# Optimization experiments

Measured on AMD Instinct MI355X. Metric: run time of the kernel, lower is better.

Reference implementation:

```python
import jax, jax.numpy as jnp
import numpy as np
from jax import lax

S = 20      # max_segments
D = 1000    # traj_dict entries
L = 200     # dmp_traj_length
CONV_OUT = 512 * 4 * 4  # 8192 for 100x100 input


def _conv(x, w, b):
    # NCHW valid conv, kernel 3x3, stride 1 (matches nn.Conv2d defaults)
    y = lax.conv_general_dilated(x, w, (1, 1), 'VALID',
                                 dimension_numbers=('NCHW', 'OIHW', 'NCHW'))
    return y + b[None, :, None, None]


def _pool2(x):
    # max_pool2d(kernel=2, stride=2), floor mode == VALID reduce_window
    return lax.reduce_window(x, -jnp.inf, lax.max, (1, 1, 2, 2), (1, 1, 2, 2), 'VALID')


def setup_inputs() -> dict:
    key = jax.random.key(0)
    ks = jax.random.split(key, 20)
    f32 = jnp.float32

    def rn(k, shape, s):
        return jax.random.normal(k, shape, dtype=f32) * s

    x = jax.random.normal(ks[0], (128, 3, 100, 100), dtype=f32)
    w1 = rn(ks[1], (64, 3, 3, 3), 0.1);    b1 = jnp.zeros((64,), f32)
    w2 = rn(ks[2], (128, 64, 3, 3), 0.04); b2 = jnp.zeros((128,), f32)
    w3 = rn(ks[3], (256, 128, 3, 3), 0.03); b3 = jnp.zeros((256,), f32)
    w4 = rn(ks[4], (512, 256, 3, 3), 0.02); b4 = jnp.zeros((512,), f32)
    out_size = 2 + 3 * S
    fw1 = rn(ks[5], (CONV_OUT, 2048), 0.01); fb1 = jnp.zeros((2048,), f32)
    fw2 = rn(ks[6], (2048, 2048), 0.02);     fb2 = jnp.zeros((2048,), f32)
    fw3 = rn(ks[7], (2048, out_size), 0.02); fb3 = jnp.zeros((out_size,), f32)
    traj_dict = jax.random.normal(ks[8], (D, L, 2), dtype=f32)
    return {
        'x': x,
        'w1': w1, 'b1': b1, 'w2': w2, 'b2': b2,
        'w3': w3, 'b3': b3, 'w4': w4, 'b4': b4,
        'fw1': fw1, 'fb1': fb1, 'fw2': fw2, 'fb2': fb2,
        'fw3': fw3, 'fb3': fb3,
        'traj_dict': traj_dict,
    }


def _forward(x, w1, b1, w2, b2, w3, b3, w4, b4,
             fw1, fb1, fw2, fb2, fw3, fb3, traj_dict):
    # conv encoder (relu(maxpool(conv)) x4, matching the torch order)
    h = jax.nn.relu(_pool2(_conv(x, w1, b1)))
    h = jax.nn.relu(_pool2(_conv(h, w2, b2)))
    h = jax.nn.relu(_pool2(_conv(h, w3, b3)))
    h = jax.nn.relu(_pool2(_conv(h, w4, b4)))
    h = h.reshape(h.shape[0], -1)                      # [B, 8192]
    # FC stack: tanh on hidden layers, linear head (dropout p=0 / eval)
    h = jnp.tanh(h @ fw1 + fb1)
    h = jnp.tanh(h @ fw2 + fb2)
    p = h @ fw3 + fb3                                  # [B, 2 + 3S]

    B = p.shape[0]
    init_pos = p[:, :2]                                # [B, 2]
    seg = p[:, 2:].reshape(B, S, 3)                    # (dict_idx, x_scale, y_scale)

    # getTrajFromDict: the loop of round/clamp/sign/abs one-hot masks is exactly
    # a gather at the clamped rounded index (round is half-to-even in both torch and jax)
    idx = jnp.clip(jnp.round(seg[..., 0]), 0, D - 1).astype(jnp.int32)  # [B, S]
    base = traj_dict[idx]                              # [B, S, L, 2]

    scaled = base * seg[:, :, None, 1:3]               # [B, S, L, 2]
    # chain segments: each segment starts at previous segment's endpoint
    offsets = scaled[:, :, -1, :]                      # [B, S, 2]
    starts = init_pos[:, None, :] + jnp.cumsum(offsets, axis=1) - offsets  # exclusive cumsum
    traj = (scaled + starts[:, :, None, :]).reshape(B, S * L, 2)
    return traj


def reference(x, w1, b1, w2, b2, w3, b3, w4, b4,
              fw1, fb1, fw2, fb2, fw3, fb3, traj_dict):
    return _forward(x, w1, b1, w2, b2, w3, b3, w4, b4,
                    fw1, fb1, fw2, fb2, fw3, fb3, traj_dict)
```

## Files before the change

### kernel.cpp

```cpp
#include <hip/hip_runtime.h>
#include <hip/hip_bf16.h>

typedef __attribute__((ext_vector_type(8))) short s8v;
typedef __attribute__((ext_vector_type(4))) float f4v;
typedef unsigned short ushort;
typedef unsigned int uint;

union V8 { s8v v; short s[8]; };

__device__ __forceinline__ short f2bf(float v){
    union { __hip_bfloat16 b; short u; } x;
    x.b = __float2bfloat16(v);
    return x.u;
}
__device__ __forceinline__ float bf2f(short u){
    union { short u; __hip_bfloat16 b; } x;
    x.u = u;
    return __bfloat162float(x.b);
}
__device__ __forceinline__ void splitf(float v, short& h, short& l){
    h = f2bf(v);
    l = f2bf(v - bf2f(h));
}
__device__ __forceinline__ uint packsplit(float v){
    short h, l; splitf(v, h, l);
    return (uint)(ushort)h | ((uint)(ushort)l << 16);
}

template<int CIN, int HIN, int PH, int OCB, int SPT, int OCS, int CICH, int COUT>
__global__ __launch_bounds__(SPT*OCS) void k_conv_pool_relu(
    const float* __restrict__ in, const float* __restrict__ w,
    const float* __restrict__ bias, uint* __restrict__ out)
{
    constexpr int BT    = SPT * OCS;
    constexpr int WIN   = HIN;
    constexpr int PW    = PH;
    constexpr int OCBLK = OCB * OCS;
    constexpr int WSTR  = CICH * 9 + 1;

    __shared__ float wsh[OCBLK * WSTR];

    const int b   = blockIdx.z;
    const int oc0 = blockIdx.y * OCBLK;
    const int t   = threadIdx.x;
    const int spl = (OCS == 1) ? t : (t % SPT);
    const int ocq = (OCS == 1) ? 0 : (t / SPT);
    const int sp  = blockIdx.x * SPT + spl;
    const bool active = sp < PH * PW;
    const int py = active ? (sp / PW) : 0;
    const int px = active ? (sp % PW) : 0;

    float acc[OCB][4];
#pragma unroll
    for (int j = 0; j < OCB; ++j)
        acc[j][0] = acc[j][1] = acc[j][2] = acc[j][3] = 0.f;

    const float* inb = in + (size_t)b * CIN * HIN * WIN;

    for (int c0 = 0; c0 < CIN; c0 += CICH) {
        __syncthreads();
        for (int i = t; i < OCBLK * CICH * 9; i += BT) {
            int j = i / (CICH * 9);
            int r = i - j * (CICH * 9);
            wsh[j * WSTR + r] = w[((size_t)(oc0 + j) * CIN + c0) * 9 + r];
        }
        __syncthreads();

        for (int ci = 0; ci < CICH; ++ci) {
            const float* inc = inb + (size_t)(c0 + ci) * HIN * WIN
                             + (2 * py) * WIN + 2 * px;
            float patch[4][4];
#pragma unroll
            for (int r = 0; r < 4; ++r)
#pragma unroll
                for (int c = 0; c < 4; ++c)
                    patch[r][c] = inc[r * WIN + c];

#pragma unroll
            for (int j = 0; j < OCB; ++j) {
                const float* wp = &wsh[(ocq * OCB + j) * WSTR + ci * 9];
#pragma unroll
                for (int kh = 0; kh < 3; ++kh)
#pragma unroll
                    for (int kw = 0; kw < 3; ++kw) {
                        float wv = wp[kh * 3 + kw];
                        acc[j][0] = fmaf(patch[kh][kw],         wv, acc[j][0]);
                        acc[j][1] = fmaf(patch[kh][kw + 1],     wv, acc[j][1]);
                        acc[j][2] = fmaf(patch[kh + 1][kw],     wv, acc[j][2]);
                        acc[j][3] = fmaf(patch[kh + 1][kw + 1], wv, acc[j][3]);
                    }
            }
        }
    }

    if (active) {
#pragma unroll
        for (int j = 0; j < OCB; ++j) {
            int oc = oc0 + ocq * OCB + j;
            float m = fmaxf(fmaxf(acc[j][0], acc[j][1]),
                            fmaxf(acc[j][2], acc[j][3]));
            m = fmaxf(m + bias[oc], 0.f);
            out[(((size_t)b * COUT + oc) * PH + py) * PW + px] = packsplit(m);
        }
    }
}

__global__ void k_wsplit_perm(const float* __restrict__ w, ushort* __restrict__ oh,
                              ushort* __restrict__ ol, int CIN, int total)
{
    int i = blockIdx.x * 256 + threadIdx.x;
    if (i < total) {
        int K = CIN * 9;
        int n = i / K;
        int rem = i - n * K;
        int ci = rem / 9;
        int r = rem - 9 * ci;
        short h, l; splitf(w[i], h, l);
        size_t o = (size_t)n * K + r * CIN + ci;
        oh[o] = (ushort)h; ol[o] = (ushort)l;
    }
}

__global__ __launch_bounds__(256) void k_wsplitT(
    const float* __restrict__ B, ushort* __restrict__ oh, ushort* __restrict__ ol,
    int K, int N)
{
    __shared__ float tl[32][33];
    const int n0 = blockIdx.x * 32, k0 = blockIdx.y * 32;
    const int r = threadIdx.x >> 5, c = threadIdx.x & 31;
#pragma unroll
    for (int it = 0; it < 4; ++it) {
        int row = r + it * 8;
        tl[row][c] = B[(size_t)(k0 + row) * N + n0 + c];
    }
    __syncthreads();
#pragma unroll
    for (int it = 0; it < 4; ++it) {
        int a = r + it * 8;
        float v = tl[c][a];
        short h, l; splitf(v, h, l);
        size_t o = (size_t)(n0 + a) * K + k0 + c;
        oh[o] = (ushort)h; ol[o] = (ushort)l;
    }
}

template<int MODE, int BPRE, int EPI, int LOG2CIN, int K, int KCH, int N,
         int HIN, int PPH, int PPW, int COUT, int TPI>
__global__ __launch_bounds__(256) void k_gemm3(
    const void* __restrict__ A0, const void* __restrict__ A1,
    const void* __restrict__ B0, const void* __restrict__ B1,
    const float* __restrict__ bias, void* __restrict__ O0, void* __restrict__ O1)
{
    constexpr int CIN = 1 << LOG2CIN;
    constexpr int HH  = HIN * HIN;

    __shared__ short Ah[64][40], Al[64][40], Bh[128][40], Bl[128][40];

    const int t    = threadIdx.x;
    const int lane = t & 63;
    const int wave = t >> 6;
    const int n0   = blockIdx.y * 128;
    const int sArow = t & 63, sAoct = t >> 6;
    const int sBrow = t & 127, sBo = t >> 7;

    const uint*   ArI = nullptr;
    const ushort* Ahg = nullptr;
    const ushort* Alg = nullptr;
    int b = 0, ptile = 0, kbeg = 0, kend = K;

    if (MODE == 0) {
        b = blockIdx.x / TPI;
        ptile = blockIdx.x - b * TPI;
        int pl = ptile * 16 + (sArow >> 2);
        int quad = sArow & 3;
        int py = 0, px = 0;
        if (pl < PPH * PPW) { py = pl / PPW; px = pl - py * PPW; }
        ArI = (const uint*)A0 + (size_t)b * CIN * HH
            + (size_t)(2 * py + (quad >> 1)) * HIN + (2 * px + (quad & 1));
    } else {
        int arow = blockIdx.x * 64 + sArow;
        Ahg = (const ushort*)A0 + (size_t)arow * K;
        Alg = (const ushort*)A1 + (size_t)arow * K;
        kbeg = blockIdx.z * KCH;
        kend = kbeg + KCH;
    }

    auto pfA = [&](int kkx, V8& ha, V8& la) {
        const int kb = kkx + sAoct * 8;
        if (MODE == 0) {
            const int r  = kb >> LOG2CIN;
            const int cb = kb & (CIN - 1);
            const int rh = (r * 11) >> 5;
            const int rw = r - 3 * rh;
            const uint* g = ArI + (size_t)cb * HH + rh * HIN + rw;
#pragma unroll
            for (int j = 0; j < 8; ++j) {
                uint v = g[(size_t)j * HH];
                ha.s[j] = (short)(v & 0xffffu);
                la.s[j] = (short)(v >> 16);
            }
        } else {
            ha.v = *(const s8v*)(Ahg + kb);
            la.v = *(const s8v*)(Alg + kb);
        }
    };
    auto pfB = [&](int kkx, V8* hb, V8* lb) {
#pragma unroll
        for (int q = 0; q < 2; ++q) {
            const int o = sBo + 2 * q;
            const int kb = kkx + o * 8;
            if (BPRE) {
                hb[q].v = *(const s8v*)((const ushort*)B0 + (size_t)(n0 + sBrow) * K + kb);
                lb[q].v = *(const s8v*)((const ushort*)B1 + (size_t)(n0 + sBrow) * K + kb);
            } else if (MODE == 0) {
                const int r  = kb >> LOG2CIN;
                const int cb = kb & (CIN - 1);
                const float* bp = (const float*)B0
                    + (size_t)(n0 + sBrow) * K + (size_t)cb * 9 + r;
#pragma unroll
                for (int j = 0; j < 8; ++j)
                    splitf(bp[9 * j], hb[q].s[j], lb[q].s[j]);
            } else {
                const float* bp = (const float*)B0 + (size_t)kb * N + n0 + sBrow;
#pragma unroll
                for (int j = 0; j < 8; ++j)
                    splitf(bp[(size_t)j * N], hb[q].s[j], lb[q].s[j]);
            }
        }
    };

    f4v acc[2][4];
    const f4v z4 = {0.f, 0.f, 0.f, 0.f};
#pragma unroll
    for (int i = 0; i < 2; ++i)
#pragma unroll
        for (int j = 0; j < 4; ++j) acc[i][j] = z4;

    V8 pAh, pAl, pBh[2], pBl[2];
    pfA(kbeg, pAh, pAl);
    pfB(kbeg, pBh, pBl);

    for (int kk = kbeg; kk < kend; kk += 32) {
        __syncthreads();
        *(s8v*)&Ah[sArow][sAoct * 8] = pAh.v;
        *(s8v*)&Al[sArow][sAoct * 8] = pAl.v;
#pragma unroll
        for (int q = 0; q < 2; ++q) {
            const int o = sBo + 2 * q;
            *(s8v*)&Bh[sBrow][o * 8] = pBh[q].v;
            *(s8v*)&Bl[sBrow][o * 8] = pBl[q].v;
        }
        if (kk + 32 < kend) {
            pfA(kk + 32, pAh, pAl);
            pfB(kk + 32, pBh, pBl);
        }
        __syncthreads();

        const int fm = lane & 15;
        const int fk = (lane >> 4) * 8;
        s8v a_h[2], a_l[2], b_h[4], b_l[4];
#pragma unroll
        for (int i = 0; i < 2; ++i) {
            a_h[i] = *(const s8v*)&Ah[(wave & 1) * 32 + i * 16 + fm][fk];
            a_l[i] = *(const s8v*)&Al[(wave & 1) * 32 + i * 16 + fm][fk];
        }
#pragma unroll
        for (int j = 0; j < 4; ++j) {
            b_h[j] = *(const s8v*)&Bh[(wave >> 1) * 64 + j * 16 + fm][fk];
            b_l[j] = *(const s8v*)&Bl[(wave >> 1) * 64 + j * 16 + fm][fk];
        }
#define MF(a_, b_, c_) c_ = __builtin_amdgcn_mfma_f32_16x16x32_bf16(a_, b_, c_, 0, 0, 0)
#pragma unroll
        for (int i = 0; i < 2; ++i)
#pragma unroll
            for (int j = 0; j < 4; ++j) {
                MF(a_h[i], b_h[j], acc[i][j]);
                MF(a_h[i], b_l[j], acc[i][j]);
                MF(a_l[i], b_h[j], acc[i][j]);
            }
#undef MF
    }

    if (MODE == 0) {
        const int PP = PPH * PPW;
#pragma unroll
        for (int i = 0; i < 2; ++i)
#pragma unroll
            for (int j = 0; j < 4; ++j) {
                int p  = ptile * 16 + (wave & 1) * 8 + i * 4 + (lane >> 4);
                int oc = n0 + (wave >> 1) * 64 + j * 16 + (lane & 15);
                if (p < PP) {
                    f4v v = acc[i][j];
                    float m = fmaxf(fmaxf(v.x, v.y), fmaxf(v.z, v.w));
                    m = fmaxf(m + bias[oc], 0.f);
                    size_t o = (size_t)(b * COUT + oc) * PP + p;
                    if (EPI == 0) {
                        ((uint*)O0)[o] = packsplit(m);
                    } else {
                        short h, l; splitf(m, h, l);
                        ((ushort*)O0)[o] = (ushort)h;
                        ((ushort*)O1)[o] = (ushort)l;
                    }
                }
            }
    } else {
        float* P = (float*)O0 + (size_t)blockIdx.z * 128 * N;
#pragma unroll
        for (int i = 0; i < 2; ++i)
#pragma unroll
            for (int j = 0; j < 4; ++j) {
                int n = n0 + (wave >> 1) * 64 + j * 16 + (lane & 15);
                int mb = blockIdx.x * 64 + (wave & 1) * 32 + i * 16 + (lane >> 4) * 4;
                f4v v = acc[i][j];
                P[(size_t)(mb + 0) * N + n] = v.x;
                P[(size_t)(mb + 1) * N + n] = v.y;
                P[(size_t)(mb + 2) * N + n] = v.z;
                P[(size_t)(mb + 3) * N + n] = v.w;
            }
    }
}

template<int EFMT>
__global__ void k_fc_epi2(const float* __restrict__ P, const float* __restrict__ bias,
                          ushort* __restrict__ oh, ushort* __restrict__ ol,
                          float* __restrict__ of, int MN, int N, int KS)
{
    int i = blockIdx.x * 256 + threadIdx.x;
    if (i >= MN) return;
    float s = 0.f;
    for (int z = 0; z < KS; ++z) s += P[(size_t)z * MN + i];
    s = tanhf(s + bias[i % N]);
    if (EFMT == 1) {
        short h, l; splitf(s, h, l);
        oh[i] = (ushort)h; ol[i] = (ushort)l;
    } else {
        of[i] = s;
    }
}

__global__ __launch_bounds__(64) void k_fc3_part(
    const float* __restrict__ A, const float* __restrict__ B,
    float* __restrict__ P, int K, int N, int KS)
{
    const int m = blockIdx.x, kz = blockIdx.y;
    const int n = threadIdx.x;
    const int kchunk = K / KS;
    if (n < N) {
        float acc = 0.f;
        const float* Am = A + (size_t)m * K;
        const int ke = (kz + 1) * kchunk;
        for (int k = kz * kchunk; k < ke; ++k)
            acc = fmaf(Am[k], B[(size_t)k * N + n], acc);
        P[((size_t)kz * 128 + m) * N + n] = acc;
    }
}

__global__ void k_fc_epi(const float* __restrict__ P, const float* __restrict__ bias,
                         float* __restrict__ out, int MN, int N, int KS)
{
    int i = blockIdx.x * 256 + threadIdx.x;
    if (i >= MN) return;
    float s = 0.f;
    for (int z = 0; z < KS; ++z) s += P[(size_t)z * MN + i];
    out[i] = s + bias[i % N];
}

__global__ void k_traj_start(const float* __restrict__ p, const float* __restrict__ td,
                             float* __restrict__ starts, float* __restrict__ sa,
                             int* __restrict__ sidx)
{
    int b = threadIdx.x;
    const float* pb = p + b * 62;
    float cx = pb[0], cy = pb[1];
    for (int s = 0; s < 20; ++s) {
        float f  = pb[2 + 3 * s];
        float a0 = pb[3 + 3 * s];
        float a1 = pb[4 + 3 * s];
        int idx = (int)fminf(fmaxf(rintf(f), 0.f), 999.f);
        int bs = b * 20 + s;
        sidx[bs] = idx;
        sa[bs * 2 + 0] = a0;
        sa[bs * 2 + 1] = a1;
        starts[bs * 2 + 0] = cx;
        starts[bs * 2 + 1] = cy;
        cx += td[((size_t)idx * 200 + 199) * 2 + 0] * a0;
        cy += td[((size_t)idx * 200 + 199) * 2 + 1] * a1;
    }
}

__global__ void k_traj_main(const float* __restrict__ td, const float* __restrict__ starts,
                            const float* __restrict__ sa, const int* __restrict__ sidx,
                            float* __restrict__ out)
{
    int bs = blockIdx.x;
    int idx = sidx[bs];
    float a0 = sa[bs * 2 + 0], a1 = sa[bs * 2 + 1];
    float s0 = starts[bs * 2 + 0], s1 = starts[bs * 2 + 1];
    const float* row = td + (size_t)idx * 400;
    float* o = out + (size_t)bs * 400;
    for (int e = threadIdx.x; e < 400; e += blockDim.x) {
        float v = row[e];
        o[e] = (e & 1) ? fmaf(v, a1, s1) : fmaf(v, a0, s0);
    }
}

template<int BPRE>
static void run_all(void* const* d_in, float* out, char* ws, hipStream_t stream)
{
    const float* x   = (const float*)d_in[0];
    const float* w1  = (const float*)d_in[1];
    const float* b1  = (const float*)d_in[2];
    const float* w2  = (const float*)d_in[3];
    const float* b2  = (const float*)d_in[4];
    const float* w3  = (const float*)d_in[5];
    const float* b3  = (const float*)d_in[6];
    const float* w4  = (const float*)d_in[7];
    const float* b4  = (const float*)d_in[8];
    const float* fw1 = (const float*)d_in[9];
    const float* fb1 = (const float*)d_in[10];
    const float* fw2 = (const float*)d_in[11];
    const float* fb2 = (const float*)d_in[12];
    const float* fw3 = (const float*)d_in[13];
    const float* fb3 = (const float*)d_in[14];
    const float* td  = (const float*)d_in[15];

    uint*   h1   = (uint*)ws;
    uint*   h2   = (uint*)(ws + 78675968ull);
    uint*   h3   = (uint*)ws;
    ushort* fw1h = (ushort*)(ws + 13107200ull);
    ushort* fw1l = (ushort*)(ws + 46661632ull);
    ushort* h4h  = (ushort*)(ws + 80216064ull);
    ushort* h4l  = (ushort*)(ws + 82313216ull);
    ushort* fw2h = (ushort*)(ws + 84410368ull);
    ushort* fw2l = (ushort*)(ws + 92798976ull);
    float*  part = (float*)(ws + 101187584ull);
    ushort* a1h  = (ushort*)(ws + 109576192ull);
    ushort* a1l  = (ushort*)(ws + 110100480ull);
    float*  a2   = (float*)(ws + 110624768ull);
    float*  p    = (float*)(ws + 111673344ull);
    float*  starts = (float*)(ws + 111705088ull);
    float*  sa   = (float*)(ws + 111725568ull);
    int*    sidx = (int*)(ws + 111746048ull);
    ushort* w2h = (ushort*)(ws + 113344512ull);
    ushort* w2l = (ushort*)(ws + 113491968ull);
    ushort* w3h = (ushort*)(ws + 113639424ull);
    ushort* w3l = (ushort*)(ws + 114229248ull);
    ushort* w4h = (ushort*)(ws + 114819072ull);
    ushort* w4l = (ushort*)(ws + 117178368ull);

    if (BPRE) {
        k_wsplit_perm<<<(73728 + 255) / 256, 256, 0, stream>>>(w2, w2h, w2l, 64, 73728);
        k_wsplit_perm<<<(294912 + 255) / 256, 256, 0, stream>>>(w3, w3h, w3l, 128, 294912);
        k_wsplit_perm<<<(1179648 + 255) / 256, 256, 0, stream>>>(w4, w4h, w4l, 256, 1179648);
    }

    k_conv_pool_relu<3, 100, 49, 16, 256, 1, 3, 64>
        <<<dim3(10, 4, 128), 256, 0, stream>>>(x, w1, b1, h1);

    k_gemm3<0, BPRE, 0, 6, 576, 576, 128, 49, 23, 23, 128, 34>
        <<<dim3(34 * 128, 1), 256, 0, stream>>>(
            h1, nullptr, BPRE ? (const void*)w2h : (const void*)w2,
            BPRE ? (const void*)w2l : nullptr, b2, h2, nullptr);
    k_gemm3<0, BPRE, 0, 7, 1152, 1152, 256, 23, 10, 10, 256, 7>
        <<<dim3(7 * 128, 2), 256, 0, stream>>>(
            h2, nullptr, BPRE ? (const void*)w3h : (const void*)w3,
            BPRE ? (const void*)w3l : nullptr, b3, h3, nullptr);

    if (BPRE) {
        k_wsplitT<<<dim3(2048 / 32, 8192 / 32), 256, 0, stream>>>(fw1, fw1h, fw1l, 8192, 2048);
        k_wsplitT<<<dim3(2048 / 32, 2048 / 32), 256, 0, stream>>>(fw2, fw2h, fw2l, 2048, 2048);
    }

    k_gemm3<0, BPRE, 1, 8, 2304, 2304, 512, 10, 4, 4, 512, 1>
        <<<dim3(128, 4), 256, 0, stream>>>(
            h3, nullptr, BPRE ? (const void*)w4h : (const void*)w4,
            BPRE ? (const void*)w4l : nullptr, b4, h4h, h4l);

    k_gemm3<1, BPRE, 2, 0, 8192, 1024, 2048, 1, 1, 1, 1, 1>
        <<<dim3(2, 16, 8), 256, 0, stream>>>(
            h4h, h4l, BPRE ? (const void*)fw1h : (const void*)fw1,
            BPRE ? (const void*)fw1l : nullptr, nullptr, part, nullptr);
    k_fc_epi2<1><<<(128 * 2048 + 255) / 256, 256, 0, stream>>>(
        part, fb1, a1h, a1l, nullptr, 128 * 2048, 2048, 8);
    k_gemm3<1, BPRE, 2, 0, 2048, 256, 2048, 1, 1, 1, 1, 1>
        <<<dim3(2, 16, 8), 256, 0, stream>>>(
            a1h, a1l, BPRE ? (const void*)fw2h : (const void*)fw2,
            BPRE ? (const void*)fw2l : nullptr, nullptr, part, nullptr);
    k_fc_epi2<2><<<(128 * 2048 + 255) / 256, 256, 0, stream>>>(
        part, fb2, nullptr, nullptr, a2, 128 * 2048, 2048, 8);

    k_fc3_part<<<dim3(128, 4), 64, 0, stream>>>(a2, fw3, part, 2048, 62, 4);
    k_fc_epi<<<(128 * 62 + 255) / 256, 256, 0, stream>>>(
        part, fb3, p, 128 * 62, 62, 4);
    k_traj_start<<<1, 128, 0, stream>>>(p, td, starts, sa, sidx);
    k_traj_main<<<2560, 256, 0, stream>>>(td, starts, sa, sidx, out);
}

extern "C" void kernel_launch(void* const* d_in, const int* in_sizes, int n_in,
                              void* d_out, int out_size, void* d_ws, size_t ws_size,
                              hipStream_t stream)
{
    (void)in_sizes; (void)n_in; (void)out_size;
    if (ws_size >= 119537664ull)
        run_all<1>(d_in, (float*)d_out, (char*)d_ws, stream);
    else
        run_all<0>(d_in, (float*)d_out, (char*)d_ws, stream);
}
```

Baseline: 1.077 ms.

## Switch intermediate conv activations to channels-last layout for vectorized im2col loads

Conv1 and the conv2/conv3 implicit-GEMM epilogues now write activations in NHWC order instead of NCHW. The im2col A-operand fetch in the GEMM then reads 8 consecutive channels with two 16-byte vector loads instead of 8 strided scalar loads. The aim is to cut the uncoalesced global-load cost of the conv GEMMs. Epilogue stores become channel-strided per thread, and conv1 drops its OCS thread-splitting option.

```diff
diff --git a/kernel.cpp b/kernel.cpp
--- a/kernel.cpp
+++ b/kernel.cpp
@@ -27,25 +27,21 @@
     return (uint)(ushort)h | ((uint)(ushort)l << 16);
 }
 
-template<int CIN, int HIN, int PH, int OCB, int SPT, int OCS, int CICH, int COUT>
-__global__ __launch_bounds__(SPT*OCS) void k_conv_pool_relu(
+template<int CIN, int HIN, int PH, int OCB, int SPT, int CICH, int COUT>
+__global__ __launch_bounds__(SPT) void k_conv_pool_relu(
     const float* __restrict__ in, const float* __restrict__ w,
     const float* __restrict__ bias, uint* __restrict__ out)
 {
-    constexpr int BT    = SPT * OCS;
     constexpr int WIN   = HIN;
     constexpr int PW    = PH;
-    constexpr int OCBLK = OCB * OCS;
     constexpr int WSTR  = CICH * 9 + 1;
 
-    __shared__ float wsh[OCBLK * WSTR];
+    __shared__ float wsh[OCB * WSTR];
 
     const int b   = blockIdx.z;
-    const int oc0 = blockIdx.y * OCBLK;
+    const int oc0 = blockIdx.y * OCB;
     const int t   = threadIdx.x;
-    const int spl = (OCS == 1) ? t : (t % SPT);
-    const int ocq = (OCS == 1) ? 0 : (t / SPT);
-    const int sp  = blockIdx.x * SPT + spl;
+    const int sp  = blockIdx.x * SPT + t;
     const bool active = sp < PH * PW;
     const int py = active ? (sp / PW) : 0;
     const int px = active ? (sp % PW) : 0;
@@ -59,7 +55,7 @@
 
     for (int c0 = 0; c0 < CIN; c0 += CICH) {
         __syncthreads();
-        for (int i = t; i < OCBLK * CICH * 9; i += BT) {
+        for (int i = t; i < OCB * CICH * 9; i += SPT) {
             int j = i / (CICH * 9);
             int r = i - j * (CICH * 9);
             wsh[j * WSTR + r] = w[((size_t)(oc0 + j) * CIN + c0) * 9 + r];
@@ -78,7 +74,7 @@
 
 #pragma unroll
             for (int j = 0; j < OCB; ++j) {
-                const float* wp = &wsh[(ocq * OCB + j) * WSTR + ci * 9];
+                const float* wp = &wsh[j * WSTR + ci * 9];
 #pragma unroll
                 for (int kh = 0; kh < 3; ++kh)
 #pragma unroll
@@ -94,14 +90,18 @@
     }
 
     if (active) {
+        uint tmp[OCB];
 #pragma unroll
         for (int j = 0; j < OCB; ++j) {
-            int oc = oc0 + ocq * OCB + j;
             float m = fmaxf(fmaxf(acc[j][0], acc[j][1]),
                             fmaxf(acc[j][2], acc[j][3]));
-            m = fmaxf(m + bias[oc], 0.f);
-            out[(((size_t)b * COUT + oc) * PH + py) * PW + px] = packsplit(m);
-        }
+            m = fmaxf(m + bias[oc0 + j], 0.f);
+            tmp[j] = packsplit(m);
+        }
+        uint* ob = out + ((size_t)b * PH * PW + sp) * COUT + oc0;
+#pragma unroll
+        for (int q = 0; q < OCB / 4; ++q)
+            ((uint4*)ob)[q] = ((const uint4*)tmp)[q];
     }
 }
 
@@ -146,7 +146,7 @@
 
 template<int MODE, int BPRE, int EPI, int LOG2CIN, int K, int KCH, int N,
          int HIN, int PPH, int PPW, int COUT, int TPI>
-__global__ __launch_bounds__(256) void k_gemm3(
+__global__ __launch_bounds__(256) void k_gemm4(
     const void* __restrict__ A0, const void* __restrict__ A1,
     const void* __restrict__ B0, const void* __restrict__ B1,
     const float* __restrict__ bias, void* __restrict__ O0, void* __restrict__ O1)
@@ -175,8 +175,9 @@
         int quad = sArow & 3;
         int py = 0, px = 0;
         if (pl < PPH * PPW) { py = pl / PPW; px = pl - py * PPW; }
-        ArI = (const uint*)A0 + (size_t)b * CIN * HH
-            + (size_t)(2 * py + (quad >> 1)) * HIN + (2 * px + (quad & 1));
+        ArI = (const uint*)A0
+            + ((size_t)b * HH + (size_t)(2 * py + (quad >> 1)) * HIN
+               + (2 * px + (quad & 1))) * CIN;
     } else {
         int arow = blockIdx.x * 64 + sArow;
         Ahg = (const ushort*)A0 + (size_t)arow * K;
@@ -192,12 +193,14 @@
             const int cb = kb & (CIN - 1);
             const int rh = (r * 11) >> 5;
             const int rw = r - 3 * rh;
-            const uint* g = ArI + (size_t)cb * HH + rh * HIN + rw;
+            const uint* g = ArI + (rh * HIN + rw) * CIN + cb;
+            uint4 v0 = *(const uint4*)g;
+            uint4 v1 = *(const uint4*)(g + 4);
+            uint vv[8] = {v0.x, v0.y, v0.z, v0.w, v1.x, v1.y, v1.z, v1.w};
 #pragma unroll
             for (int j = 0; j < 8; ++j) {
-                uint v = g[(size_t)j * HH];
-                ha.s[j] = (short)(v & 0xffffu);
-                la.s[j] = (short)(v >> 16);
+                ha.s[j] = (short)(vv[j] & 0xffffu);
+                la.s[j] = (short)(vv[j] >> 16);
             }
         } else {
             ha.v = *(const s8v*)(Ahg + kb);
@@ -293,10 +296,10 @@
                     f4v v = acc[i][j];
                     float m = fmaxf(fmaxf(v.x, v.y), fmaxf(v.z, v.w));
                     m = fmaxf(m + bias[oc], 0.f);
-                    size_t o = (size_t)(b * COUT + oc) * PP + p;
                     if (EPI == 0) {
-                        ((uint*)O0)[o] = packsplit(m);
+                        ((uint*)O0)[((size_t)b * PP + p) * COUT + oc] = packsplit(m);
                     } else {
+                        size_t o = (size_t)(b * COUT + oc) * PP + p;
                         short h, l; splitf(m, h, l);
                         ((ushort*)O0)[o] = (ushort)h;
                         ((ushort*)O1)[o] = (ushort)l;
@@ -454,14 +457,14 @@
         k_wsplit_perm<<<(1179648 + 255) / 256, 256, 0, stream>>>(w4, w4h, w4l, 256, 1179648);
     }
 
-    k_conv_pool_relu<3, 100, 49, 16, 256, 1, 3, 64>
+    k_conv_pool_relu<3, 100, 49, 16, 256, 3, 64>
         <<<dim3(10, 4, 128), 256, 0, stream>>>(x, w1, b1, h1);
 
-    k_gemm3<0, BPRE, 0, 6, 576, 576, 128, 49, 23, 23, 128, 34>
+    k_gemm4<0, BPRE, 0, 6, 576, 576, 128, 49, 23, 23, 128, 34>
         <<<dim3(34 * 128, 1), 256, 0, stream>>>(
             h1, nullptr, BPRE ? (const void*)w2h : (const void*)w2,
             BPRE ? (const void*)w2l : nullptr, b2, h2, nullptr);
-    k_gemm3<0, BPRE, 0, 7, 1152, 1152, 256, 23, 10, 10, 256, 7>
+    k_gemm4<0, BPRE, 0, 7, 1152, 1152, 256, 23, 10, 10, 256, 7>
         <<<dim3(7 * 128, 2), 256, 0, stream>>>(
             h2, nullptr, BPRE ? (const void*)w3h : (const void*)w3,
             BPRE ? (const void*)w3l : nullptr, b3, h3, nullptr);
@@ -471,18 +474,18 @@
         k_wsplitT<<<dim3(2048 / 32, 2048 / 32), 256, 0, stream>>>(fw2, fw2h, fw2l, 2048, 2048);
     }
 
-    k_gemm3<0, BPRE, 1, 8, 2304, 2304, 512, 10, 4, 4, 512, 1>
+    k_gemm4<0, BPRE, 1, 8, 2304, 2304, 512, 10, 4, 4, 512, 1>
         <<<dim3(128, 4), 256, 0, stream>>>(
             h3, nullptr, BPRE ? (const void*)w4h : (const void*)w4,
             BPRE ? (const void*)w4l : nullptr, b4, h4h, h4l);
 
-    k_gemm3<1, BPRE, 2, 0, 8192, 1024, 2048, 1, 1, 1, 1, 1>
+    k_gemm4<1, BPRE, 2, 0, 8192, 1024, 2048, 1, 1, 1, 1, 1>
         <<<dim3(2, 16, 8), 256, 0, stream>>>(
             h4h, h4l, BPRE ? (const void*)fw1h : (const void*)fw1,
             BPRE ? (const void*)fw1l : nullptr, nullptr, part, nullptr);
     k_fc_epi2<1><<<(128 * 2048 + 255) / 256, 256, 0, stream>>>(
         part, fb1, a1h, a1l, nullptr, 128 * 2048, 2048, 8);
-    k_gemm3<1, BPRE, 2, 0, 2048, 256, 2048, 1, 1, 1, 1, 1>
+    k_gemm4<1, BPRE, 2, 0, 2048, 256, 2048, 1, 1, 1, 1, 1>
         <<<dim3(2, 16, 8), 256, 0, stream>>>(
             a1h, a1l, BPRE ? (const void*)fw2h : (const void*)fw2,
             BPRE ? (const void*)fw2l : nullptr, nullptr, part, nullptr);
```

After: 1.045 ms. 3.0% less time.
